# Optimization experiments

Hardware: AMD Instinct MI355X
Metric: run time of the kernel (lower is better)

## Reference

```python
import jax, jax.numpy as jnp
import numpy as np

EPS_DIV = 1e-6    # safe_div clamp
EPS_NORM = 1e-12  # F.normalize eps
EPS_PD = 1e-6     # F.pairwise_distance eps (added to the difference)


def setup_inputs() -> dict:
    key = jax.random.key(0)
    k1, k2, k3 = jax.random.split(key, 3)
    B, N, D, C = 8, 2048, 512, 8192
    x = jax.random.normal(k1, (B, N, D), dtype=jnp.float32)
    W = jax.random.normal(k2, (D, D), dtype=jnp.float32) * (1.0 / np.sqrt(D))
    codebook = jax.random.normal(k3, (C, D), dtype=jnp.float32)
    return {"x": x, "W": W, "codebook": codebook}


def reference(x, W, codebook):
    sg = jax.lax.stop_gradient
    # implicit codebook = Linear(dim, dim, bias=False)(codebook)  -> codebook @ W^T
    imp = codebook @ W.T                                  # [C, D]

    lead = x.shape[:-1]
    D = x.shape[-1]
    xf = x.reshape(-1, D)                                 # [T, D]

    # nearest-neighbor search (no_grad in original): squared-dist argmin == cdist argmin
    d2 = (jnp.sum(xf * xf, axis=-1, keepdims=True)
          - 2.0 * (xf @ imp.T)
          + jnp.sum(imp * imp, axis=-1)[None, :])         # [T, C]
    indices = jnp.argmin(sg(d2), axis=-1)                 # [T]

    qf = imp[indices]                                     # [T, D] gather

    # commit loss: (pairwise_distance(x, q.detach())**2).mean(); torch adds eps to the diff
    diff = xf - sg(qf) + EPS_PD
    commit_loss = jnp.mean(jnp.sum(diff * diff, axis=-1))

    # rotation trick
    norm_x = jnp.linalg.norm(xf, axis=-1, keepdims=True)  # [T, 1]
    norm_q = jnp.linalg.norm(qf, axis=-1, keepdims=True)
    u = xf / jnp.maximum(norm_x, EPS_DIV)
    q = qf / jnp.maximum(norm_q, EPS_DIV)
    s = u + q
    w = sg(s / jnp.maximum(jnp.linalg.norm(s, axis=-1, keepdims=True), EPS_NORM))
    e = xf
    # e - 2 (e.w) w + 2 (e.u_sg) q_sg   (rank-1 products per row)
    rot = (e
           - 2.0 * jnp.sum(e * w, axis=-1, keepdims=True) * w
           + 2.0 * jnp.sum(e * sg(u), axis=-1, keepdims=True) * sg(q))
    quantized = rot * sg(norm_q / jnp.maximum(norm_x, EPS_DIV))

    quantized = quantized.reshape(*lead, D)
    indices = indices.reshape(*lead)
    return quantized, indices, commit_loss
```

## Files before the change

### kernel.cpp

```cpp
#include <hip/hip_runtime.h>
#include <cstdint>
#include <cstddef>

#define DD 512
#define TT 16384
#define CC 8192
#define SPLITC 32
#define EPS_DIV 1e-6f
#define EPS_NORM 1e-12f
#define EPS_PD 1e-6f

typedef _Float16 half8 __attribute__((ext_vector_type(8)));
typedef _Float16 half4 __attribute__((ext_vector_type(4)));
typedef float floatx4 __attribute__((ext_vector_type(4)));

#define GLDS16(g, l) __builtin_amdgcn_global_load_lds( \
    (const __attribute__((address_space(1))) void*)(g), \
    (__attribute__((address_space(3))) void*)(l), 16, 0, 0)

__global__ __launch_bounds__(128) void k_split(const float* __restrict__ src,
                                               _Float16* __restrict__ dst) {
  const int row = blockIdx.x;
  const int col = threadIdx.x * 4;
  float4 v = *(const float4*)(src + (size_t)row * DD + col);
  half4 h, l;
  h.x = (_Float16)v.x; l.x = (_Float16)(v.x - (float)h.x);
  h.y = (_Float16)v.y; l.y = (_Float16)(v.y - (float)h.y);
  h.z = (_Float16)v.z; l.z = (_Float16)(v.z - (float)h.z);
  h.w = (_Float16)v.w; l.w = (_Float16)(v.w - (float)h.w);
  *(half4*)(dst + (size_t)row * 1024 + col) = h;
  *(half4*)(dst + (size_t)row * 1024 + 512 + col) = l;
}

__global__ __launch_bounds__(128) void k_cast16(const float* __restrict__ src,
                                                _Float16* __restrict__ dst) {
  const int row = blockIdx.x;
  const int col = threadIdx.x * 4;
  float4 v = *(const float4*)(src + (size_t)row * DD + col);
  half4 h;
  h.x = (_Float16)v.x; h.y = (_Float16)v.y;
  h.z = (_Float16)v.z; h.w = (_Float16)v.w;
  *(half4*)(dst + (size_t)row * DD + col) = h;
}

__global__ __launch_bounds__(256) void k_gemm_mfma(
    const _Float16* __restrict__ cbs, const _Float16* __restrict__ Ws,
    float* __restrict__ imp, _Float16* __restrict__ ih) {
  __shared__ __align__(16) char smem[65536];
  const int tid = threadIdx.x;
  const int w = tid >> 6, lane = tid & 63;
  const int quad = lane >> 4, l15 = lane & 15;
  const int wm = (w & 1) * 64, wn = (w >> 1) * 64;
  const int c0 = blockIdx.x * 128;
  const int n0 = blockIdx.y * 128;

  const int srow8 = lane >> 3;
  const int scol = ((lane & 7) ^ srow8) << 3;
  size_t arow[4], brow[4];
#pragma unroll
  for (int j = 0; j < 4; ++j) {
    arow[j] = (size_t)(c0 + j * 32 + w * 8 + srow8) * 1024 + scol;
    brow[j] = (size_t)(n0 + j * 32 + w * 8 + srow8) * 1024 + scol;
  }
  int aoff[4], boff[4];
#pragma unroll
  for (int i = 0; i < 4; ++i) {
    aoff[i] = ((wm + i * 16 + l15) * 64 + ((quad ^ (l15 & 7)) << 3)) * 2;
    boff[i] = ((wn + i * 16 + l15) * 64 + ((quad ^ (l15 & 7)) << 3)) * 2;
  }

  auto stage = [&](int buf, int ak, int bk) {
    char* ab = smem + buf * 32768;
    char* bb = ab + 16384;
#pragma unroll
    for (int j = 0; j < 4; ++j) {
      GLDS16(cbs + arow[j] + ak, (_Float16*)ab + (j * 32 + w * 8) * 64);
      GLDS16(Ws  + brow[j] + bk, (_Float16*)bb + (j * 32 + w * 8) * 64);
    }
  };

  floatx4 acc[4][4] = {};
  stage(0, 0, 0);
#pragma unroll 2
  for (int it = 0; it < 24; ++it) {
    __syncthreads();
    if (it < 23) {
      const int n = it + 1;
      const int p = n >> 3, kk = n & 7;
      const int ak = ((p == 2) ? 512 : 0) + kk * 64;
      const int bk = ((p == 1) ? 512 : 0) + kk * 64;
      stage(n & 1, ak, bk);
    }
    const char* ab = smem + (it & 1) * 32768;
    const char* bb = ab + 16384;
#pragma unroll
    for (int ks = 0; ks < 2; ++ks) {
      const int kx = ks * 64;
      half8 a[4], b[4];
#pragma unroll
      for (int mi = 0; mi < 4; ++mi)
        a[mi] = *(const half8*)(ab + (aoff[mi] ^ kx));
#pragma unroll
      for (int ni = 0; ni < 4; ++ni)
        b[ni] = *(const half8*)(bb + (boff[ni] ^ kx));
#pragma unroll
      for (int mi = 0; mi < 4; ++mi)
#pragma unroll
        for (int ni = 0; ni < 4; ++ni)
          acc[mi][ni] = __builtin_amdgcn_mfma_f32_16x16x32_f16(
              a[mi], b[ni], acc[mi][ni], 0, 0, 0);
    }
  }
#pragma unroll
  for (int mi = 0; mi < 4; ++mi)
#pragma unroll
    for (int r = 0; r < 4; ++r) {
      const int c = c0 + wm + mi * 16 + quad * 4 + r;
#pragma unroll
      for (int ni = 0; ni < 4; ++ni) {
        const int d = n0 + wn + ni * 16 + l15;
        const float v = acc[mi][ni][r];
        imp[(size_t)c * DD + d] = v;
        ih[(size_t)c * DD + d] = (_Float16)v;
      }
    }
}

__global__ __launch_bounds__(256) void k_row_norm2(
    const float* __restrict__ imp, float* __restrict__ cnorm) {
  const int lane = threadIdx.x & 63;
  const int row = blockIdx.x * 4 + (threadIdx.x >> 6);
  const float* p = imp + (size_t)row * DD + lane * 8;
  float4 a = *(const float4*)p;
  float4 b = *(const float4*)(p + 4);
  float s = a.x * a.x + a.y * a.y + a.z * a.z + a.w * a.w +
            b.x * b.x + b.y * b.y + b.z * b.z + b.w * b.w;
#pragma unroll
  for (int m = 1; m < 64; m <<= 1) s += __shfl_xor(s, m);
  if (lane == 0) cnorm[row] = s;
}

__global__ __launch_bounds__(512, 2) void k_dist_top2(
    const _Float16* __restrict__ xh, const _Float16* __restrict__ ih,
    const float* __restrict__ cnorm,
    float* __restrict__ bval, int* __restrict__ bidx) {
  __shared__ __align__(16) char smem[131072];
  const int tid = threadIdx.x;
  const int w = tid >> 6, lane = tid & 63;
  const int quad = lane >> 4, l15 = lane & 15;
  const int wr = w >> 2, wc = w & 3;
  const int r0 = blockIdx.x * 256;
  const int c0 = blockIdx.y * 256;

  const int rloc = lane >> 2;
  const int chunk = (lane & 3) ^ (rloc & 3) ^ ((rloc >> 2) & 3);
  const _Float16* pA0 = xh + (size_t)(r0 + w * 32 + rloc) * DD + chunk * 8;
  const _Float16* pA1 = pA0 + (size_t)16 * DD;
  const _Float16* pB0 = ih + (size_t)(c0 + w * 32 + rloc) * DD + chunk * 8;
  const _Float16* pB1 = pB0 + (size_t)16 * DD;
  const int ldsA0 = (w * 32) * 64;
  const int ldsA1 = ldsA0 + 16 * 64;
  const int ldsB0 = 16384 + ldsA0;
  const int ldsB1 = 16384 + ldsA1;

  const int slot = (quad ^ (l15 & 3) ^ ((l15 >> 2) & 3)) << 4;
  int aoff[8], boff[4];
#pragma unroll
  for (int mi = 0; mi < 8; ++mi)
    aoff[mi] = (wr * 128 + mi * 16 + l15) * 64 + slot;
#pragma unroll
  for (int ni = 0; ni < 4; ++ni)
    boff[ni] = 16384 + (wc * 64 + ni * 16 + l15) * 64 + slot;

  float cn[4];
#pragma unroll
  for (int ni = 0; ni < 4; ++ni)
    cn[ni] = cnorm[c0 + wc * 64 + ni * 16 + l15];

  floatx4 acc[8][4] = {};

  auto STAGE = [&](int t) {
    char* base = smem + (t & 3) * 32768;
    const size_t ko = (size_t)(t * 32);
    GLDS16(pA0 + ko, base + ldsA0);
    GLDS16(pA1 + ko, base + ldsA1);
    GLDS16(pB0 + ko, base + ldsB0);
    GLDS16(pB1 + ko, base + ldsB1);
  };
  auto COMPUTE = [&](int t) {
    const char* ab = smem + (t & 3) * 32768;
    half8 a[8], b[4];
#pragma unroll
    for (int mi = 0; mi < 8; ++mi) a[mi] = *(const half8*)(ab + aoff[mi]);
#pragma unroll
    for (int ni = 0; ni < 4; ++ni) b[ni] = *(const half8*)(ab + boff[ni]);
    asm volatile("s_waitcnt lgkmcnt(0)" ::: "memory");
    __builtin_amdgcn_sched_barrier(0);
    __builtin_amdgcn_s_barrier();
    __builtin_amdgcn_sched_barrier(0);
    __builtin_amdgcn_s_setprio(1);
#pragma unroll
    for (int mi = 0; mi < 8; ++mi)
#pragma unroll
      for (int ni = 0; ni < 4; ++ni)
        acc[mi][ni] = __builtin_amdgcn_mfma_f32_16x16x32_f16(
            a[mi], b[ni], acc[mi][ni], 0, 0, 0);
    __builtin_amdgcn_s_setprio(0);
  };

  STAGE(0); STAGE(1); STAGE(2);
#pragma unroll 1
  for (int t = 0; t < 13; ++t) {
    STAGE(t + 3);
    asm volatile("s_waitcnt vmcnt(12)" ::: "memory");
    __builtin_amdgcn_s_barrier();
    __builtin_amdgcn_sched_barrier(0);
    COMPUTE(t);
  }
  asm volatile("s_waitcnt vmcnt(8)" ::: "memory");
  __builtin_amdgcn_s_barrier();
  __builtin_amdgcn_sched_barrier(0);
  COMPUTE(13);
  asm volatile("s_waitcnt vmcnt(4)" ::: "memory");
  __builtin_amdgcn_s_barrier();
  __builtin_amdgcn_sched_barrier(0);
  COMPUTE(14);
  asm volatile("s_waitcnt vmcnt(0)" ::: "memory");
  __builtin_amdgcn_s_barrier();
  __builtin_amdgcn_sched_barrier(0);
  COMPUTE(15);

  __syncthreads();
  float* rv = (float*)smem;
  int* ri = (int*)(smem + 65536);
#pragma unroll
  for (int mi = 0; mi < 8; ++mi)
#pragma unroll
    for (int r = 0; r < 4; ++r) {
      const int row = wr * 128 + mi * 16 + quad * 4 + r;
      float bv = 3.4e38f; int bi = 0x7fffffff;
#pragma unroll
      for (int ni = 0; ni < 4; ++ni) {
        const float v = fmaf(-2.0f, acc[mi][ni][r], cn[ni]);
        const int c = c0 + wc * 64 + ni * 16 + l15;
        if (v < bv) { bv = v; bi = c; }
      }
      const int e = wc * 16 + l15;
      const int col = e ^ (row & 31);
      rv[row * 64 + col] = bv;
      ri[row * 64 + col] = bi;
    }
  __syncthreads();
  {
    const int row = tid >> 1, h = tid & 1;
    float v1 = 3.4e38f, v2 = 3.4e38f;
    int i1 = 0x7fffffff, i2 = 0x7fffffff;
#pragma unroll
    for (int j = 0; j < 32; ++j) {
      const int e = h * 32 + j;
      const int col = e ^ (row & 31);
      const float v = rv[row * 64 + col];
      const int i = ri[row * 64 + col];
      if (v < v1 || (v == v1 && i < i1)) { v2 = v1; i2 = i1; v1 = v; i1 = i; }
      else if (v < v2 || (v == v2 && i < i2)) { v2 = v; i2 = i; }
    }
    const float w1 = __shfl_xor(v1, 1), w2 = __shfl_xor(v2, 1);
    const int j1 = __shfl_xor(i1, 1), j2 = __shfl_xor(i2, 1);
    if (w1 < v1 || (w1 == v1 && j1 < i1)) {
      if (v1 < w2 || (v1 == w2 && i1 < j2)) { v2 = v1; i2 = i1; }
      else { v2 = w2; i2 = j2; }
      v1 = w1; i1 = j1;
    } else if (w1 < v2 || (w1 == v2 && j1 < i2)) { v2 = w1; i2 = j1; }
    if (h == 0) {
      const size_t o = ((size_t)blockIdx.y * TT + r0 + row) * 2;
      bval[o] = v1; bval[o + 1] = v2;
      bidx[o] = i1; bidx[o + 1] = i2;
    }
  }
}

__global__ __launch_bounds__(256) void k_epilogue(
    const float* __restrict__ x, const float* __restrict__ imp,
    const float* __restrict__ cnorm,
    const float* __restrict__ bval, const int* __restrict__ bidx,
    float* __restrict__ outq, float* __restrict__ outidx,
    float* __restrict__ rloss) {
  const int lane = threadIdx.x & 63;
  const int row = blockIdx.x * 4 + (threadIdx.x >> 6);
  float v1 = 3.4e38f, v2 = 3.4e38f;
  int i1 = 0x7fffffff, i2 = 0x7fffffff;
  if (lane < SPLITC) {
    const size_t o = ((size_t)lane * TT + row) * 2;
    v1 = bval[o]; v2 = bval[o + 1];
    i1 = bidx[o]; i2 = bidx[o + 1];
  }
#pragma unroll
  for (int m = 1; m < 64; m <<= 1) {
    const float w1 = __shfl_xor(v1, m), w2 = __shfl_xor(v2, m);
    const int j1 = __shfl_xor(i1, m), j2 = __shfl_xor(i2, m);
    if (w1 < v1 || (w1 == v1 && j1 < i1)) {
      if (v1 < w2 || (v1 == w2 && i1 < j2)) { v2 = v1; i2 = i1; }
      else { v2 = w2; i2 = j2; }
      v1 = w1; i1 = j1;
    } else {
      if (w1 < v2 || (w1 == v2 && j1 < i2)) { v2 = w1; i2 = j1; }
    }
  }
  const float* xr = x + (size_t)row * DD + lane * 8;
  float e[8], qa[8], qb[8];
  *(float4*)&e[0] = *(const float4*)xr;
  *(float4*)&e[4] = *(const float4*)(xr + 4);
  const float* q1p = imp + (size_t)i1 * DD + lane * 8;
  const float* q2p = imp + (size_t)i2 * DD + lane * 8;
  *(float4*)&qa[0] = *(const float4*)q1p;
  *(float4*)&qa[4] = *(const float4*)(q1p + 4);
  *(float4*)&qb[0] = *(const float4*)q2p;
  *(float4*)&qb[4] = *(const float4*)(q2p + 4);
  float d1 = 0.f, d2 = 0.f;
#pragma unroll
  for (int k = 0; k < 8; ++k) {
    d1 = fmaf(e[k], qa[k], d1);
    d2 = fmaf(e[k], qb[k], d2);
  }
#pragma unroll
  for (int m = 1; m < 64; m <<= 1) {
    d1 += __shfl_xor(d1, m);
    d2 += __shfl_xor(d2, m);
  }
  const float s1 = fmaf(-2.0f, d1, cnorm[i1]);
  const float s2 = fmaf(-2.0f, d2, cnorm[i2]);
  const bool use2 = (s2 < s1) || (s2 == s1 && i2 < i1);
  const int idx = use2 ? i2 : i1;
  float q[8];
#pragma unroll
  for (int k = 0; k < 8; ++k) q[k] = use2 ? qb[k] : qa[k];

  float xx = 0.f, qq = 0.f, xq = 0.f, cl = 0.f;
#pragma unroll
  for (int k = 0; k < 8; ++k) {
    xx = fmaf(e[k], e[k], xx);
    qq = fmaf(q[k], q[k], qq);
    xq = fmaf(e[k], q[k], xq);
    float d = e[k] - q[k] + EPS_PD;
    cl = fmaf(d, d, cl);
  }
#pragma unroll
  for (int m = 1; m < 64; m <<= 1) {
    xx += __shfl_xor(xx, m);
    qq += __shfl_xor(qq, m);
    xq += __shfl_xor(xq, m);
    cl += __shfl_xor(cl, m);
  }
  const float nx = sqrtf(xx), nq = sqrtf(qq);
  const float dx = fmaxf(nx, EPS_DIV), dq = fmaxf(nq, EPS_DIV);
  const float uu = xx / (dx * dx);
  const float qq2 = qq / (dq * dq);
  const float uq = xq / (dx * dq);
  const float ss = uu + qq2 + 2.0f * uq;
  const float dn = fmaxf(sqrtf(ss), EPS_NORM);
  const float es = xx / dx + xq / dq;
  const float a = 2.0f * es / (dn * dn);
  const float b = 2.0f * (xx / dx);
  const float scale = nq / dx;

  float ov[8];
#pragma unroll
  for (int k = 0; k < 8; ++k) {
    const float qp = q[k] / dq;
    const float sk = e[k] / dx + qp;
    ov[k] = (e[k] - a * sk + b * qp) * scale;
  }
  float* op = outq + (size_t)row * DD + lane * 8;
  *(float4*)op = *(const float4*)&ov[0];
  *(float4*)(op + 4) = *(const float4*)&ov[4];
  if (lane == 0) {
    outidx[row] = (float)idx;
    rloss[row] = cl;
  }
}

__global__ __launch_bounds__(256) void k_loss_final(
    const float* __restrict__ rloss, float* __restrict__ out) {
  __shared__ double red[256];
  const int tid = threadIdx.x;
  double s = 0.0;
  for (int i = tid; i < TT; i += 256) s += (double)rloss[i];
  red[tid] = s;
  __syncthreads();
  for (int st = 128; st > 0; st >>= 1) {
    if (tid < st) red[tid] += red[tid + st];
    __syncthreads();
  }
  if (tid == 0) out[0] = (float)(red[0] / (double)TT);
}

extern "C" void kernel_launch(void* const* d_in, const int* in_sizes, int n_in,
                              void* d_out, int out_size, void* d_ws, size_t ws_size,
                              hipStream_t stream) {
  const float* x  = (const float*)d_in[0];
  const float* W  = (const float*)d_in[1];
  const float* cb = (const float*)d_in[2];
  float* out = (float*)d_out;

  float* imp = (float*)d_ws;
  _Float16* ih = (_Float16*)(imp + (size_t)CC * DD);
  _Float16* cbs = ih + (size_t)CC * DD;
  _Float16* xh = cbs;
  _Float16* Ws = cbs + (size_t)CC * 1024;
  float* cnorm = (float*)(Ws + (size_t)DD * 1024);
  float* bval  = cnorm + CC;
  int*   bidx  = (int*)(bval + (size_t)SPLITC * TT * 2);
  float* rloss = (float*)(bidx + (size_t)SPLITC * TT * 2);

  float* out_q    = out;
  float* out_idx  = out + (size_t)TT * DD;
  float* out_loss = out_idx + TT;

  k_split<<<CC, 128, 0, stream>>>(cb, cbs);
  k_split<<<DD, 128, 0, stream>>>(W, Ws);
  k_gemm_mfma<<<dim3(CC / 128, DD / 128), 256, 0, stream>>>(cbs, Ws, imp, ih);
  k_row_norm2<<<CC / 4, 256, 0, stream>>>(imp, cnorm);
  k_cast16<<<TT, 128, 0, stream>>>(x, xh);
  k_dist_top2<<<dim3(TT / 256, CC / 256), 512, 0, stream>>>(xh, ih, cnorm, bval, bidx);
  k_epilogue<<<TT / 4, 256, 0, stream>>>(x, imp, cnorm, bval, bidx, out_q, out_idx, rloss);
  k_loss_final<<<1, 256, 0, stream>>>(rloss, out_loss);
}
```

Measured before the change: 343.3 us.

## Software-pipeline LDS fragment reads with MFMA and tweak epilogue LDS swizzle

Restructures the main GEMM loop so LDS reads of the next k-step's A and B fragments are interleaved with the current step's MFMAs, using double-buffered B registers and a fully unrolled macro sequence. This removes the per-iteration wait for all LDS reads to finish before the MFMA burst starts. The epilogue's swizzle pattern for the reduction scratch buffer is also changed to reduce bank conflicts. The change raises register pressure, since it holds an extra B fragment set and unrolls the whole loop, and it relies on a barrier ordering that keeps the 4-stage buffer ring safe.

```diff
diff --git a/kernel.cpp b/kernel.cpp
--- a/kernel.cpp
+++ b/kernel.cpp
@@ -178,6 +178,7 @@
     cn[ni] = cnorm[c0 + wc * 64 + ni * 16 + l15];
 
   floatx4 acc[8][4] = {};
+  half8 a[8], bX[4], bY[4];
 
   auto STAGE = [&](int t) {
     char* base = smem + (t & 3) * 32768;
@@ -187,48 +188,62 @@
     GLDS16(pB0 + ko, base + ldsB0);
     GLDS16(pB1 + ko, base + ldsB1);
   };
-  auto COMPUTE = [&](int t) {
-    const char* ab = smem + (t & 3) * 32768;
-    half8 a[8], b[4];
-#pragma unroll
-    for (int mi = 0; mi < 8; ++mi) a[mi] = *(const half8*)(ab + aoff[mi]);
-#pragma unroll
-    for (int ni = 0; ni < 4; ++ni) b[ni] = *(const half8*)(ab + boff[ni]);
-    asm volatile("s_waitcnt lgkmcnt(0)" ::: "memory");
-    __builtin_amdgcn_sched_barrier(0);
-    __builtin_amdgcn_s_barrier();
-    __builtin_amdgcn_sched_barrier(0);
-    __builtin_amdgcn_s_setprio(1);
-#pragma unroll
-    for (int mi = 0; mi < 8; ++mi)
-#pragma unroll
-      for (int ni = 0; ni < 4; ++ni)
-        acc[mi][ni] = __builtin_amdgcn_mfma_f32_16x16x32_f16(
-            a[mi], b[ni], acc[mi][ni], 0, 0, 0);
-    __builtin_amdgcn_s_setprio(0);
-  };
 
   STAGE(0); STAGE(1); STAGE(2);
-#pragma unroll 1
-  for (int t = 0; t < 13; ++t) {
-    STAGE(t + 3);
-    asm volatile("s_waitcnt vmcnt(12)" ::: "memory");
-    __builtin_amdgcn_s_barrier();
-    __builtin_amdgcn_sched_barrier(0);
-    COMPUTE(t);
-  }
   asm volatile("s_waitcnt vmcnt(8)" ::: "memory");
   __builtin_amdgcn_s_barrier();
   __builtin_amdgcn_sched_barrier(0);
-  COMPUTE(13);
-  asm volatile("s_waitcnt vmcnt(4)" ::: "memory");
-  __builtin_amdgcn_s_barrier();
-  __builtin_amdgcn_sched_barrier(0);
-  COMPUTE(14);
-  asm volatile("s_waitcnt vmcnt(0)" ::: "memory");
-  __builtin_amdgcn_s_barrier();
-  __builtin_amdgcn_sched_barrier(0);
-  COMPUTE(15);
+  {
+    const char* ab = smem;
+#pragma unroll
+    for (int mi = 0; mi < 8; ++mi) a[mi] = *(const half8*)(ab + aoff[mi]);
+#pragma unroll
+    for (int ni = 0; ni < 4; ++ni) bX[ni] = *(const half8*)(ab + boff[ni]);
+  }
+
+#define K_ITER(T, BCUR, BNXT, DO_STAGE, VMC, DO_READ)                          \
+  {                                                                            \
+    if (DO_STAGE) STAGE((T) + 3);                                              \
+    asm volatile("s_waitcnt vmcnt(" #VMC ")" ::: "memory");                    \
+    __builtin_amdgcn_s_barrier();                                              \
+    __builtin_amdgcn_sched_barrier(0);                                         \
+    asm volatile("s_waitcnt lgkmcnt(0)" ::: "memory");                         \
+    __builtin_amdgcn_sched_barrier(0);                                         \
+    const char* nb = smem + (((T) + 1) & 3) * 32768;                           \
+    __builtin_amdgcn_s_setprio(1);                                             \
+    _Pragma("unroll")                                                          \
+    for (int mi = 0; mi < 8; ++mi) {                                           \
+      _Pragma("unroll")                                                        \
+      for (int ni = 0; ni < 4; ++ni)                                           \
+        acc[mi][ni] = __builtin_amdgcn_mfma_f32_16x16x32_f16(                  \
+            a[mi], BCUR[ni], acc[mi][ni], 0, 0, 0);                            \
+      if (DO_READ) a[mi] = *(const half8*)(nb + aoff[mi]);                     \
+    }                                                                          \
+    if (DO_READ) {                                                             \
+      _Pragma("unroll")                                                        \
+      for (int ni = 0; ni < 4; ++ni)                                           \
+        BNXT[ni] = *(const half8*)(nb + boff[ni]);                             \
+    }                                                                          \
+    __builtin_amdgcn_s_setprio(0);                                             \
+  }
+
+  K_ITER(0,  bX, bY, true,  8, true)
+  K_ITER(1,  bY, bX, true,  8, true)
+  K_ITER(2,  bX, bY, true,  8, true)
+  K_ITER(3,  bY, bX, true,  8, true)
+  K_ITER(4,  bX, bY, true,  8, true)
+  K_ITER(5,  bY, bX, true,  8, true)
+  K_ITER(6,  bX, bY, true,  8, true)
+  K_ITER(7,  bY, bX, true,  8, true)
+  K_ITER(8,  bX, bY, true,  8, true)
+  K_ITER(9,  bY, bX, true,  8, true)
+  K_ITER(10, bX, bY, true,  8, true)
+  K_ITER(11, bY, bX, true,  8, true)
+  K_ITER(12, bX, bY, true,  8, true)
+  K_ITER(13, bY, bX, false, 4, true)
+  K_ITER(14, bX, bY, false, 0, true)
+  K_ITER(15, bY, bX, false, 0, false)
+#undef K_ITER
 
   __syncthreads();
   float* rv = (float*)smem;
@@ -246,19 +261,21 @@
         if (v < bv) { bv = v; bi = c; }
       }
       const int e = wc * 16 + l15;
-      const int col = e ^ (row & 31);
+      const int g = (row & 31) ^ ((row & 4) << 2);
+      const int col = e ^ g;
       rv[row * 64 + col] = bv;
       ri[row * 64 + col] = bi;
     }
   __syncthreads();
   {
     const int row = tid >> 1, h = tid & 1;
+    const int g = (row & 31) ^ ((row & 4) << 2);
     float v1 = 3.4e38f, v2 = 3.4e38f;
     int i1 = 0x7fffffff, i2 = 0x7fffffff;
 #pragma unroll
     for (int j = 0; j < 32; ++j) {
       const int e = h * 32 + j;
-      const int col = e ^ (row & 31);
+      const int col = e ^ g;
       const float v = rv[row * 64 + col];
       const int i = ri[row * 64 + col];
       if (v < v1 || (v == v1 && i < i1)) { v2 = v1; i2 = i1; v1 = v; i1 = i; }
```

Measured after the change: 343.9 us. No clear change (+0.2%).
